# Performance work log

Hardware: AMD Instinct MI355X
Metric: run time of the kernel (lower is better)

The kernel has to match this reference:

```python
import jax, jax.numpy as jnp
import numpy as np

B, T, D = 8, 1024, 128
TEMP = 0.1
WEIGHT = 1.0


def _neg_scaled_l2(x, y):
    # x: [P, T, D], y: [P, S, D] -> -||x-y||^2 / D / TEMP  (l2 similarity, normalize_dimension=True)
    x2 = jnp.sum(x * x, axis=-1)[..., :, None]            # [P, T, 1]
    y2 = jnp.sum(y * y, axis=-1)[..., None, :]            # [P, 1, S]
    xy = jnp.einsum('ptd,psd->pts', x, y)                 # [P, T, S]
    d2 = jnp.maximum(x2 + y2 - 2.0 * xy, 0.0)             # cdist(...)**2 is non-negative
    return -d2 / D / TEMP


def setup_inputs() -> dict:
    key = jax.random.key(0)
    k1, k2, k3 = jax.random.split(key, 3)
    embs = jax.random.normal(k1, (B, T, D), dtype=jnp.float32)
    frame_idxs = jnp.sort(jax.random.randint(k2, (B, T), 0, 4096, dtype=jnp.int32), axis=-1)
    video_len = jax.random.randint(k3, (B,), T, 4096, dtype=jnp.int32)
    return {"embs": embs, "frame_idxs": frame_idxs, "video_len": video_len}


def reference(embs, frame_idxs, video_len):
    # All ordered pairs (i, j) with i != j, built at trace time.
    pairs = np.array([(i, j) for i in range(B) for j in range(B) if i != j])
    ii, jj = pairs[:, 0], pairs[:, 1]                     # [P]

    e1 = embs[ii]                                         # [P, T, D]
    e2 = embs[jj]                                         # [P, T, D]

    # Cycle: soft nearest neighbors of e1 in e2, then align back to e1.
    sim12 = _neg_scaled_l2(e1, e2)                        # [P, T, T]
    beta12 = jax.nn.softmax(sim12, axis=-1)
    nn_embs = jnp.einsum('pts,psd->ptd', beta12, e2)      # [P, T, D]
    logits = _neg_scaled_l2(nn_embs, e1)                  # [P, T, T]

    beta = jax.nn.softmax(logits, axis=-1)                # [P, T, T]
    steps = frame_idxs.astype(jnp.float32) / video_len.astype(jnp.float32)[:, None]  # [B, T]
    sp = steps[ii]                                        # [P, T] (steps of sequence i)
    time_true = sp                                        # one_hot(labels) picks the diagonal
    time_pred = jnp.einsum('pts,ps->pt', beta, sp)        # [P, T]
    loss = jnp.mean((time_pred - time_true) ** 2)
    return WEIGHT * loss
```

## Files before the change

### kernel.cpp

```cpp
#include <hip/hip_runtime.h>
#include <hip/hip_bf16.h>


#define T_ 1024
#define D_ 128
#define NPAIR 56
#define NSCALE 0.11271055006945026f
#define SQDS 0.474785316f

typedef float f32x16 __attribute__((ext_vector_type(16)));

#define B8F 131072
#define B8T 163840

__device__ __forceinline__ unsigned short f2bf(float f) {
  unsigned u = __float_as_uint(f);
  u += 0x7fff + ((u >> 16) & 1);
  return (unsigned short)(u >> 16);
}
__device__ __forceinline__ float bf2f(unsigned short v) {
  return __uint_as_float(((unsigned)v) << 16);
}
__device__ __forceinline__ float clamp8(float x) {
  return fminf(fmaxf(x, -440.f), 440.f);
}
__device__ __forceinline__ unsigned pk4(float a, float b, float c, float d) {
  int w = __builtin_amdgcn_cvt_pk_fp8_f32(a, b, 0, false);
  w = __builtin_amdgcn_cvt_pk_fp8_f32(c, d, w, true);
  return (unsigned)w;
}
__device__ __forceinline__ float waveSum(float v) {
#pragma unroll
  for (int k = 32; k >= 1; k >>= 1) v += __shfl_xor(v, k, 64);
  return v;
}

__device__ __forceinline__ void c2b8(const unsigned* m, int lh, long long* b0, long long* b1) {
  unsigned send0 = lh ? m[0] : m[1];
  unsigned send1 = lh ? m[2] : m[3];
  unsigned r0 = (unsigned)__shfl_xor((int)send0, 32, 64);
  unsigned r1 = (unsigned)__shfl_xor((int)send1, 32, 64);
  union { unsigned u[2]; long long ll; } x0, x1;
  x0.u[0] = lh ? r0 : m[0];  x0.u[1] = lh ? m[1] : r0;
  x1.u[0] = lh ? r1 : m[2];  x1.u[1] = lh ? m[3] : r1;
  *b0 = x0.ll; *b1 = x1.ll;
}

#define MFMA8(A, B, C) __builtin_amdgcn_mfma_f32_32x32x16_fp8_fp8((A), (B), (C), 0, 0, 0)
#define LD8(P, Q) (*(const long long*)((P) + (Q) * 512))
#define EXPC(x) fminf(__builtin_amdgcn_exp2f(x), 448.f)

__global__ __launch_bounds__(256) void convert_kernel(
    const float* __restrict__ embs, const int* __restrict__ fi,
    const int* __restrict__ vl, unsigned char* __restrict__ e8F,
    unsigned char* __restrict__ e8T, float* __restrict__ steps,
    float* __restrict__ acc, unsigned* __restrict__ cnt) {
  __shared__ unsigned short tileS[32 * 136];
  __shared__ float psum[32][8];
  __shared__ float g_sh[32], sp_sh[32];
  const int b = blockIdx.x >> 5;
  const int t0 = (blockIdx.x & 31) * 32;
  const int tid = threadIdx.x;
  const int row = tid >> 3, seg = tid & 7;

  if (blockIdx.x == 0 && tid == 0) { acc[0] = 0.f; cnt[0] = 0u; }

  const float* src = embs + (size_t)(b * T_ + t0 + row) * D_ + seg * 16;
  float4 g4[4];
#pragma unroll
  for (int k = 0; k < 4; k++) g4[k] = ((const float4*)src)[k];
  float s = 0.f;
  float fv[16];
#pragma unroll
  for (int k = 0; k < 4; k++) {
    s += g4[k].x * g4[k].x + g4[k].y * g4[k].y + g4[k].z * g4[k].z + g4[k].w * g4[k].w;
    fv[4 * k + 0] = g4[k].x * SQDS; fv[4 * k + 1] = g4[k].y * SQDS;
    fv[4 * k + 2] = g4[k].z * SQDS; fv[4 * k + 3] = g4[k].w * SQDS;
  }
  psum[row][seg] = s;

  {
    unsigned char* dstA = e8F + (size_t)b * B8F + (size_t)((t0 >> 5) * 8 + seg) * 512;
    uint2 lo, hi;
    lo.x = pk4(fv[0], fv[1], fv[2], fv[3]);   lo.y = pk4(fv[4], fv[5], fv[6], fv[7]);
    hi.x = pk4(fv[8], fv[9], fv[10], fv[11]); hi.y = pk4(fv[12], fv[13], fv[14], fv[15]);
    *(uint2*)(dstA + row * 8) = lo;
    *(uint2*)(dstA + (size_t)(32 + row) * 8) = hi;
  }
#pragma unroll
  for (int k = 0; k < 16; k++) tileS[row * 136 + seg * 16 + k] = f2bf(fv[k]);
  __syncthreads();

  if (tid < 32) {
    float t = 0.f;
#pragma unroll
    for (int k = 0; k < 8; k++) t += psum[tid][k];
    int gr = b * T_ + t0 + tid;
    float sp = (float)fi[gr] / (float)vl[b];
    steps[gr] = sp;
    sp_sh[tid] = sp;
    g_sh[tid] = __builtin_amdgcn_exp2f(14.0f - t * NSCALE);
  }
  __syncthreads();

  {
    const int c8 = tid >> 5;
    const int n2 = c8 & 3, scp = c8 >> 2;
    const int dd = n2 * 32 + (tid & 31);
#pragma unroll
    for (int half = 0; half < 2; half++) {
      const int lane = half * 32 + (tid & 31);
      const int sl = scp * 16 + half * 8;
      float vv[8];
#pragma unroll
      for (int jj = 0; jj < 8; jj++)
        vv[jj] = clamp8(bf2f(tileS[(sl + jj) * 136 + dd]) * g_sh[sl + jj]);
      uint2 wv;
      wv.x = pk4(vv[0], vv[1], vv[2], vv[3]);
      wv.y = pk4(vv[4], vv[5], vv[6], vv[7]);
      int c = n2 * 64 + (t0 >> 4) + scp;
      *(uint2*)(e8T + (size_t)b * B8T + (size_t)c * 512 + lane * 8) = wv;
    }
  }
  if (tid < 128) {
    const int sc2 = tid >> 6, lane = tid & 63;
    const int m = lane & 31, kh = lane >> 5;
    uint2 wv; wv.x = 0u; wv.y = 0u;
    if (m < 2) {
      float vv[8];
#pragma unroll
      for (int e = 0; e < 8; e++) {
        int sl = sc2 * 16 + kh * 8 + e;
        float gg = g_sh[sl];
        vv[e] = clamp8(m ? gg * sp_sh[sl] : gg);
      }
      wv.x = pk4(vv[0], vv[1], vv[2], vv[3]);
      wv.y = pk4(vv[4], vv[5], vv[6], vv[7]);
    }
    int c = 256 + (t0 >> 4) + sc2;
    *(uint2*)(e8T + (size_t)b * B8T + (size_t)c * 512 + lane * 8) = wv;
  }
}

__global__ __launch_bounds__(256, 2) void tcc_main(
    const unsigned char* __restrict__ e8F, const unsigned char* __restrict__ e8T,
    const float* __restrict__ steps, float* __restrict__ loss_acc,
    unsigned* __restrict__ cnt, float* __restrict__ out) {
  __shared__ float blred[4];

  const int bx = blockIdx.x;
  const int pair = bx >> 3;
  const int tile = bx & 7;
  const int i = pair / 7;
  const int r = pair % 7;
  const int j = r + (r >= i ? 1 : 0);
  const int tid = threadIdx.x;
  const int w = tid >> 6;
  const int l = tid & 63;
  const int l31 = l & 31;
  const int lh = l >> 5;
  const int tb = tile * 128 + w * 32;

  const unsigned char* eFi = e8F + (size_t)i * B8F;
  const unsigned char* eFj = e8F + (size_t)j * B8F;
  const unsigned char* eTj = e8T + (size_t)j * B8T;
  const unsigned char* eTi = e8T + (size_t)i * B8T;

  long long qf8[8];
  {
    const unsigned char* qb = eFi + (size_t)((tb >> 5) * 8) * 512 + l * 8;
#pragma unroll
    for (int kc = 0; kc < 8; kc++) qf8[kc] = LD8(qb, kc);
  }

  const f32x16 Z = {0.f, 0.f, 0.f, 0.f, 0.f, 0.f, 0.f, 0.f,
                    0.f, 0.f, 0.f, 0.f, 0.f, 0.f, 0.f, 0.f};
  const f32x16 CM6 = {-6.f, -6.f, -6.f, -6.f, -6.f, -6.f, -6.f, -6.f,
                      -6.f, -6.f, -6.f, -6.f, -6.f, -6.f, -6.f, -6.f};
  f32x16 o[5];
#pragma unroll
  for (int n2 = 0; n2 < 5; n2++) o[n2] = Z;

  for (int st = 0; st < 16; st++) {
    const unsigned char* kb = eFj + (size_t)(st * 16) * 512 + l * 8;
    const unsigned char* vb = eTj + (size_t)(st * 4) * 512 + l * 8;

    f32x16 ca0 = MFMA8(LD8(kb, 0), qf8[0], CM6);
    f32x16 ca1 = MFMA8(LD8(kb, 8), qf8[0], CM6);
#pragma unroll
    for (int dc = 1; dc < 8; dc++) {
      ca0 = MFMA8(LD8(kb, dc), qf8[dc], ca0);
      ca1 = MFMA8(LD8(kb, 8 + dc), qf8[dc], ca1);
    }
    unsigned m0[4], m1[4];
#pragma unroll
    for (int k2 = 0; k2 < 4; k2++) {
      m0[k2] = pk4(EXPC(ca0[4 * k2]), EXPC(ca0[4 * k2 + 1]),
                   EXPC(ca0[4 * k2 + 2]), EXPC(ca0[4 * k2 + 3]));
      m1[k2] = pk4(EXPC(ca1[4 * k2]), EXPC(ca1[4 * k2 + 1]),
                   EXPC(ca1[4 * k2 + 2]), EXPC(ca1[4 * k2 + 3]));
    }
    long long pB[4];
    c2b8(m0, lh, &pB[0], &pB[1]);
    c2b8(m1, lh, &pB[2], &pB[3]);
#pragma unroll
    for (int n2 = 0; n2 < 5; n2++)
#pragma unroll
      for (int sc = 0; sc < 4; sc++)
        o[n2] = MFMA8(LD8(vb, n2 * 64 + sc), pB[sc], o[n2]);
  }

  float Lme = o[4][0];
  float Lo = __shfl_xor(Lme, 32, 64);
  float inv = 1.0f / (lh ? Lo : Lme);
  long long qf2[8];
#pragma unroll
  for (int n2 = 0; n2 < 4; n2++) {
    unsigned mm[4];
#pragma unroll
    for (int k2 = 0; k2 < 4; k2++)
      mm[k2] = pk4(o[n2][4 * k2] * inv, o[n2][4 * k2 + 1] * inv,
                   o[n2][4 * k2 + 2] * inv, o[n2][4 * k2 + 3] * inv);
    c2b8(mm, lh, &qf2[2 * n2], &qf2[2 * n2 + 1]);
  }
  f32x16 acc6 = Z;

  for (int st = 0; st < 16; st++) {
    const unsigned char* kb = eFi + (size_t)(st * 16) * 512 + l * 8;
    const unsigned char* gb = eTi + (size_t)(256 + st * 4) * 512 + l * 8;

    f32x16 ca0 = MFMA8(LD8(kb, 0), qf2[0], CM6);
    f32x16 ca1 = MFMA8(LD8(kb, 8), qf2[0], CM6);
#pragma unroll
    for (int dc = 1; dc < 8; dc++) {
      ca0 = MFMA8(LD8(kb, dc), qf2[dc], ca0);
      ca1 = MFMA8(LD8(kb, 8 + dc), qf2[dc], ca1);
    }
    unsigned m0[4], m1[4];
#pragma unroll
    for (int k2 = 0; k2 < 4; k2++) {
      m0[k2] = pk4(EXPC(ca0[4 * k2]), EXPC(ca0[4 * k2 + 1]),
                   EXPC(ca0[4 * k2 + 2]), EXPC(ca0[4 * k2 + 3]));
      m1[k2] = pk4(EXPC(ca1[4 * k2]), EXPC(ca1[4 * k2 + 1]),
                   EXPC(ca1[4 * k2 + 2]), EXPC(ca1[4 * k2 + 3]));
    }
    long long pB[4];
    c2b8(m0, lh, &pB[0], &pB[1]);
    c2b8(m1, lh, &pB[2], &pB[3]);
#pragma unroll
    for (int sc = 0; sc < 4; sc++)
      acc6 = MFMA8(LD8(gb, sc), pB[sc], acc6);
  }

  float local = 0.f;
  if (lh == 0) {
    float pred = acc6[1] / acc6[0];
    float tt = steps[i * T_ + tb + l31];
    float dd = pred - tt;
    local = dd * dd;
  }
  local = waveSum(local);
  if (l == 0) blred[w] = local;
  __syncthreads();
  if (tid == 0) {
    atomicAdd(loss_acc, blred[0] + blred[1] + blred[2] + blred[3]);
    __threadfence();
    unsigned old = atomicAdd(cnt, 1u);
    if (old == (unsigned)(gridDim.x - 1)) {
      float v = atomicAdd(loss_acc, 0.0f);
      out[0] = v * (1.0f / (float)(NPAIR * T_));
    }
  }
}

extern "C" void kernel_launch(void* const* d_in, const int* in_sizes, int n_in,
                              void* d_out, int out_size, void* d_ws, size_t ws_size,
                              hipStream_t stream) {
  const float* embs = (const float*)d_in[0];
  const int* frame_idxs = (const int*)d_in[1];
  const int* video_len = (const int*)d_in[2];
  float* out = (float*)d_out;

  char* ws = (char*)d_ws;
  float* acc = (float*)ws;
  unsigned* cnt = (unsigned*)(ws + 512);
  float* steps = (float*)(ws + 4096);
  unsigned char* e8F = (unsigned char*)(ws + 65536);
  unsigned char* e8T = e8F + (size_t)8 * B8F;

  convert_kernel<<<dim3(256), dim3(256), 0, stream>>>(embs, frame_idxs, video_len,
                                                      e8F, e8T, steps, acc, cnt);
  tcc_main<<<dim3(NPAIR * 8), dim3(256), 0, stream>>>(e8F, e8T, steps, acc, cnt, out);
}
```

Baseline: 133.7 us.

## Use single-wave blocks with double-buffered async global-to-LDS staging of K/V tiles

Moves from 4-wave blocks to one wave per block (4x more blocks) and stages the fp8 key/value tiles into LDS through global_load_lds with a two-deep buffer and manual vmcnt waits, so loads overlap with MFMA and exp work. Each iteration now handles 32 keys instead of 64, and the block reduction through shared memory becomes a per-wave atomic. The cost is more atomics, hand-written waitcnt accounting that is fragile, and 18KB of LDS per single-wave block, which may limit occupancy.

New measurement: 141.3 us. 1.06x slower.

```diff
diff --git a/kernel.cpp b/kernel.cpp
--- a/kernel.cpp
+++ b/kernel.cpp
@@ -33,6 +33,11 @@
 #pragma unroll
   for (int k = 32; k >= 1; k >>= 1) v += __shfl_xor(v, k, 64);
   return v;
+}
+__device__ __forceinline__ void stage1k(const unsigned char* g, unsigned char* lds, int lane) {
+  __builtin_amdgcn_global_load_lds(
+      (const __attribute__((address_space(1))) unsigned int*)(g + lane * 16),
+      (__attribute__((address_space(3))) unsigned int*)lds, 16, 0, 0);
 }
 
 __device__ __forceinline__ void c2b8(const unsigned* m, int lh, long long* b0, long long* b1) {
@@ -49,6 +54,8 @@
 #define MFMA8(A, B, C) __builtin_amdgcn_mfma_f32_32x32x16_fp8_fp8((A), (B), (C), 0, 0, 0)
 #define LD8(P, Q) (*(const long long*)((P) + (Q) * 512))
 #define EXPC(x) fminf(__builtin_amdgcn_exp2f(x), 448.f)
+#define WAITV(N) asm volatile("s_waitcnt vmcnt(" #N ")" ::: "memory")
+#define WAITL() asm volatile("s_waitcnt lgkmcnt(0)" ::: "memory")
 
 __global__ __launch_bounds__(256) void convert_kernel(
     const float* __restrict__ embs, const int* __restrict__ fi,
@@ -142,24 +149,22 @@
   }
 }
 
-__global__ __launch_bounds__(256, 2) void tcc_main(
+__global__ __launch_bounds__(64) void tcc_main(
     const unsigned char* __restrict__ e8F, const unsigned char* __restrict__ e8T,
     const float* __restrict__ steps, float* __restrict__ loss_acc,
     unsigned* __restrict__ cnt, float* __restrict__ out) {
-  __shared__ float blred[4];
+  __shared__ unsigned char smem[18432];
 
   const int bx = blockIdx.x;
-  const int pair = bx >> 3;
-  const int tile = bx & 7;
+  const int pair = bx >> 5;
+  const int tile = bx & 31;
   const int i = pair / 7;
   const int r = pair % 7;
   const int j = r + (r >= i ? 1 : 0);
-  const int tid = threadIdx.x;
-  const int w = tid >> 6;
-  const int l = tid & 63;
+  const int l = threadIdx.x & 63;
   const int l31 = l & 31;
   const int lh = l >> 5;
-  const int tb = tile * 128 + w * 32;
+  const int tb = tile * 32;
 
   const unsigned char* eFi = e8F + (size_t)i * B8F;
   const unsigned char* eFj = e8F + (size_t)j * B8F;
@@ -168,7 +173,7 @@
 
   long long qf8[8];
   {
-    const unsigned char* qb = eFi + (size_t)((tb >> 5) * 8) * 512 + l * 8;
+    const unsigned char* qb = eFi + (size_t)(tile * 8) * 512 + l * 8;
 #pragma unroll
     for (int kc = 0; kc < 8; kc++) qf8[kc] = LD8(qb, kc);
   }
@@ -181,34 +186,59 @@
 #pragma unroll
   for (int n2 = 0; n2 < 5; n2++) o[n2] = Z;
 
-  for (int st = 0; st < 16; st++) {
-    const unsigned char* kb = eFj + (size_t)(st * 16) * 512 + l * 8;
-    const unsigned char* vb = eTj + (size_t)(st * 4) * 512 + l * 8;
-
-    f32x16 ca0 = MFMA8(LD8(kb, 0), qf8[0], CM6);
-    f32x16 ca1 = MFMA8(LD8(kb, 8), qf8[0], CM6);
-#pragma unroll
-    for (int dc = 1; dc < 8; dc++) {
-      ca0 = MFMA8(LD8(kb, dc), qf8[dc], ca0);
-      ca1 = MFMA8(LD8(kb, 8 + dc), qf8[dc], ca1);
-    }
-    unsigned m0[4], m1[4];
-#pragma unroll
-    for (int k2 = 0; k2 < 4; k2++) {
-      m0[k2] = pk4(EXPC(ca0[4 * k2]), EXPC(ca0[4 * k2 + 1]),
-                   EXPC(ca0[4 * k2 + 2]), EXPC(ca0[4 * k2 + 3]));
-      m1[k2] = pk4(EXPC(ca1[4 * k2]), EXPC(ca1[4 * k2 + 1]),
-                   EXPC(ca1[4 * k2 + 2]), EXPC(ca1[4 * k2 + 3]));
-    }
-    long long pB[4];
+  auto stg1 = [&](int t, int b) {
+    unsigned char* dst = smem + b * 9216;
+#pragma unroll
+    for (int u = 0; u < 4; u++)
+      stage1k(eFj + ((size_t)t * 8 + u * 2) * 512, dst + u * 1024, l);
+#pragma unroll
+    for (int n2 = 0; n2 < 4; n2++)
+      stage1k(eTj + ((size_t)n2 * 64 + t * 2) * 512, dst + 4096 + n2 * 1024, l);
+    stage1k(eTj + ((size_t)256 + t * 2) * 512, dst + 4096 + 4096, l);
+  };
+  auto stg2 = [&](int t, int b) {
+    unsigned char* dst = smem + b * 9216;
+#pragma unroll
+    for (int u = 0; u < 4; u++)
+      stage1k(eFi + ((size_t)t * 8 + u * 2) * 512, dst + u * 1024, l);
+    stage1k(eTi + ((size_t)256 + t * 2) * 512, dst + 4096, l);
+  };
+
+  stg1(0, 0);
+  stg1(1, 1);
+
+  for (int st = 0; st < 32; st++) {
+    const int buf = st & 1;
+    if (st == 31) { WAITV(0); } else { WAITV(9); }
+
+    const unsigned char* kb = smem + buf * 9216 + l * 8;
+    const unsigned char* vb = kb + 4096;
+
+    f32x16 ca = MFMA8(LD8(kb, 0), qf8[0], CM6);
+#pragma unroll
+    for (int dc = 1; dc < 8; dc++) ca = MFMA8(LD8(kb, dc), qf8[dc], ca);
+    unsigned m0[4];
+#pragma unroll
+    for (int k2 = 0; k2 < 4; k2++)
+      m0[k2] = pk4(EXPC(ca[4 * k2]), EXPC(ca[4 * k2 + 1]),
+                   EXPC(ca[4 * k2 + 2]), EXPC(ca[4 * k2 + 3]));
+    long long pB[2];
     c2b8(m0, lh, &pB[0], &pB[1]);
-    c2b8(m1, lh, &pB[2], &pB[3]);
 #pragma unroll
     for (int n2 = 0; n2 < 5; n2++)
 #pragma unroll
-      for (int sc = 0; sc < 4; sc++)
-        o[n2] = MFMA8(LD8(vb, n2 * 64 + sc), pB[sc], o[n2]);
-  }
+      for (int sc = 0; sc < 2; sc++)
+        o[n2] = MFMA8(LD8(vb, n2 * 2 + sc), pB[sc], o[n2]);
+
+    if (st < 30) {
+      WAITL();
+      stg1(st + 2, buf);
+    }
+  }
+
+  WAITL();
+  stg2(0, 0);
+  stg2(1, 1);
 
   float Lme = o[4][0];
   float Lo = __shfl_xor(Lme, 32, 64);
@@ -225,31 +255,31 @@
   }
   f32x16 acc6 = Z;
 
-  for (int st = 0; st < 16; st++) {
-    const unsigned char* kb = eFi + (size_t)(st * 16) * 512 + l * 8;
-    const unsigned char* gb = eTi + (size_t)(256 + st * 4) * 512 + l * 8;
-
-    f32x16 ca0 = MFMA8(LD8(kb, 0), qf2[0], CM6);
-    f32x16 ca1 = MFMA8(LD8(kb, 8), qf2[0], CM6);
-#pragma unroll
-    for (int dc = 1; dc < 8; dc++) {
-      ca0 = MFMA8(LD8(kb, dc), qf2[dc], ca0);
-      ca1 = MFMA8(LD8(kb, 8 + dc), qf2[dc], ca1);
-    }
-    unsigned m0[4], m1[4];
-#pragma unroll
-    for (int k2 = 0; k2 < 4; k2++) {
-      m0[k2] = pk4(EXPC(ca0[4 * k2]), EXPC(ca0[4 * k2 + 1]),
-                   EXPC(ca0[4 * k2 + 2]), EXPC(ca0[4 * k2 + 3]));
-      m1[k2] = pk4(EXPC(ca1[4 * k2]), EXPC(ca1[4 * k2 + 1]),
-                   EXPC(ca1[4 * k2 + 2]), EXPC(ca1[4 * k2 + 3]));
-    }
-    long long pB[4];
+  for (int st = 0; st < 32; st++) {
+    const int buf = st & 1;
+    if (st == 31) { WAITV(0); } else { WAITV(5); }
+
+    const unsigned char* kb = smem + buf * 9216 + l * 8;
+    const unsigned char* gb = kb + 4096;
+
+    f32x16 da = MFMA8(LD8(kb, 0), qf2[0], CM6);
+#pragma unroll
+    for (int dc = 1; dc < 8; dc++) da = MFMA8(LD8(kb, dc), qf2[dc], da);
+    unsigned m0[4];
+#pragma unroll
+    for (int k2 = 0; k2 < 4; k2++)
+      m0[k2] = pk4(EXPC(da[4 * k2]), EXPC(da[4 * k2 + 1]),
+                   EXPC(da[4 * k2 + 2]), EXPC(da[4 * k2 + 3]));
+    long long pB[2];
     c2b8(m0, lh, &pB[0], &pB[1]);
-    c2b8(m1, lh, &pB[2], &pB[3]);
-#pragma unroll
-    for (int sc = 0; sc < 4; sc++)
+#pragma unroll
+    for (int sc = 0; sc < 2; sc++)
       acc6 = MFMA8(LD8(gb, sc), pB[sc], acc6);
+
+    if (st < 30) {
+      WAITL();
+      stg2(st + 2, buf);
+    }
   }
 
   float local = 0.f;
@@ -260,10 +290,8 @@
     local = dd * dd;
   }
   local = waveSum(local);
-  if (l == 0) blred[w] = local;
-  __syncthreads();
-  if (tid == 0) {
-    atomicAdd(loss_acc, blred[0] + blred[1] + blred[2] + blred[3]);
+  if (l == 0) {
+    atomicAdd(loss_acc, local);
     __threadfence();
     unsigned old = atomicAdd(cnt, 1u);
     if (old == (unsigned)(gridDim.x - 1)) {
@@ -290,5 +318,5 @@
 
   convert_kernel<<<dim3(256), dim3(256), 0, stream>>>(embs, frame_idxs, video_len,
                                                       e8F, e8T, steps, acc, cnt);
-  tcc_main<<<dim3(NPAIR * 8), dim3(256), 0, stream>>>(e8F, e8T, steps, acc, cnt, out);
-}
+  tcc_main<<<dim3(NPAIR * 32), dim3(64), 0, stream>>>(e8F, e8T, steps, acc, cnt, out);
+}
```

## Stage K/V tiles into LDS with async double-buffered global_load_lds

Applied to the files above, without the earlier changes.

Main kernel now uses 128-thread blocks covering 64 query rows, doubling the grid. Key and value fp8 tiles are copied from global memory straight into a double-buffered LDS region with global_load_lds, prefetching the next step while the current one computes. MFMA sections are wrapped in setprio hints. This aims to hide global load latency and let the two waves share staged tiles, at the cost of a per-step __syncthreads, 36KB of LDS per block, and twice as many blocks reloading the same K/V data.

Measured after the change: 122.8 us. 8.2% less time.

```diff
diff --git a/kernel.cpp b/kernel.cpp
--- a/kernel.cpp
+++ b/kernel.cpp
@@ -33,6 +33,11 @@
 #pragma unroll
   for (int k = 32; k >= 1; k >>= 1) v += __shfl_xor(v, k, 64);
   return v;
+}
+__device__ __forceinline__ void stage1k(const unsigned char* g, unsigned char* lds, int lane) {
+  __builtin_amdgcn_global_load_lds(
+      (const __attribute__((address_space(1))) unsigned int*)(g + lane * 16),
+      (__attribute__((address_space(3))) unsigned int*)lds, 16, 0, 0);
 }
 
 __device__ __forceinline__ void c2b8(const unsigned* m, int lh, long long* b0, long long* b1) {
@@ -142,15 +147,19 @@
   }
 }
 
-__global__ __launch_bounds__(256, 2) void tcc_main(
+__global__ __launch_bounds__(128, 2) void tcc_main(
     const unsigned char* __restrict__ e8F, const unsigned char* __restrict__ e8T,
     const float* __restrict__ steps, float* __restrict__ loss_acc,
     unsigned* __restrict__ cnt, float* __restrict__ out) {
-  __shared__ float blred[4];
+  __shared__ unsigned char smem[36864];
+  __shared__ float blred[2];
+  unsigned char* kt = smem;
+  unsigned char* vt = smem + 16384;
+  unsigned char* gt = smem + 16384;
 
   const int bx = blockIdx.x;
-  const int pair = bx >> 3;
-  const int tile = bx & 7;
+  const int pair = bx >> 4;
+  const int tile = bx & 15;
   const int i = pair / 7;
   const int r = pair % 7;
   const int j = r + (r >= i ? 1 : 0);
@@ -159,7 +168,7 @@
   const int l = tid & 63;
   const int l31 = l & 31;
   const int lh = l >> 5;
-  const int tb = tile * 128 + w * 32;
+  const int tb = tile * 64 + w * 32;
 
   const unsigned char* eFi = e8F + (size_t)i * B8F;
   const unsigned char* eFj = e8F + (size_t)j * B8F;
@@ -181,10 +190,36 @@
 #pragma unroll
   for (int n2 = 0; n2 < 5; n2++) o[n2] = Z;
 
+  auto stageP1 = [&](int t, int b) {
+#pragma unroll
+    for (int q = 0; q < 4; q++)
+      stage1k(eFj + (size_t)(8 * t + 4 * w + q) * 1024, kt + b * 8192 + (4 * w + q) * 1024, l);
+#pragma unroll
+    for (int u = 0; u < 5; u++) {
+      int vu = w + 2 * u;
+      int n2v = vu >> 1, uh = vu & 1;
+      stage1k(eTj + (size_t)(n2v * 32 + t * 2 + uh) * 1024, vt + b * 10240 + vu * 1024, l);
+    }
+  };
+  auto stageP2 = [&](int t, int b) {
+#pragma unroll
+    for (int q = 0; q < 4; q++)
+      stage1k(eFi + (size_t)(8 * t + 4 * w + q) * 1024, kt + b * 8192 + (4 * w + q) * 1024, l);
+    stage1k(eTi + (size_t)(128 + t * 2 + w) * 1024, gt + b * 2048 + w * 1024, l);
+  };
+
+  stageP1(0, 0);
+  __syncthreads();
+
   for (int st = 0; st < 16; st++) {
-    const unsigned char* kb = eFj + (size_t)(st * 16) * 512 + l * 8;
-    const unsigned char* vb = eTj + (size_t)(st * 4) * 512 + l * 8;
-
+    const int cur = st & 1, nxt = cur ^ 1;
+    if (st < 15) stageP1(st + 1, nxt);
+    __builtin_amdgcn_sched_barrier(0);
+
+    const unsigned char* kb = kt + cur * 8192 + l * 8;
+    const unsigned char* vb = vt + cur * 10240 + l * 8;
+
+    __builtin_amdgcn_s_setprio(1);
     f32x16 ca0 = MFMA8(LD8(kb, 0), qf8[0], CM6);
     f32x16 ca1 = MFMA8(LD8(kb, 8), qf8[0], CM6);
 #pragma unroll
@@ -192,6 +227,7 @@
       ca0 = MFMA8(LD8(kb, dc), qf8[dc], ca0);
       ca1 = MFMA8(LD8(kb, 8 + dc), qf8[dc], ca1);
     }
+    __builtin_amdgcn_s_setprio(0);
     unsigned m0[4], m1[4];
 #pragma unroll
     for (int k2 = 0; k2 < 4; k2++) {
@@ -203,12 +239,17 @@
     long long pB[4];
     c2b8(m0, lh, &pB[0], &pB[1]);
     c2b8(m1, lh, &pB[2], &pB[3]);
+    __builtin_amdgcn_s_setprio(1);
 #pragma unroll
     for (int n2 = 0; n2 < 5; n2++)
 #pragma unroll
       for (int sc = 0; sc < 4; sc++)
-        o[n2] = MFMA8(LD8(vb, n2 * 64 + sc), pB[sc], o[n2]);
-  }
+        o[n2] = MFMA8(LD8(vb, n2 * 4 + sc), pB[sc], o[n2]);
+    __builtin_amdgcn_s_setprio(0);
+    __syncthreads();
+  }
+
+  stageP2(0, 0);
 
   float Lme = o[4][0];
   float Lo = __shfl_xor(Lme, 32, 64);
@@ -224,11 +265,17 @@
     c2b8(mm, lh, &qf2[2 * n2], &qf2[2 * n2 + 1]);
   }
   f32x16 acc6 = Z;
+  __syncthreads();
 
   for (int st = 0; st < 16; st++) {
-    const unsigned char* kb = eFi + (size_t)(st * 16) * 512 + l * 8;
-    const unsigned char* gb = eTi + (size_t)(256 + st * 4) * 512 + l * 8;
-
+    const int cur = st & 1, nxt = cur ^ 1;
+    if (st < 15) stageP2(st + 1, nxt);
+    __builtin_amdgcn_sched_barrier(0);
+
+    const unsigned char* kb = kt + cur * 8192 + l * 8;
+    const unsigned char* gb = gt + cur * 2048 + l * 8;
+
+    __builtin_amdgcn_s_setprio(1);
     f32x16 ca0 = MFMA8(LD8(kb, 0), qf2[0], CM6);
     f32x16 ca1 = MFMA8(LD8(kb, 8), qf2[0], CM6);
 #pragma unroll
@@ -236,6 +283,7 @@
       ca0 = MFMA8(LD8(kb, dc), qf2[dc], ca0);
       ca1 = MFMA8(LD8(kb, 8 + dc), qf2[dc], ca1);
     }
+    __builtin_amdgcn_s_setprio(0);
     unsigned m0[4], m1[4];
 #pragma unroll
     for (int k2 = 0; k2 < 4; k2++) {
@@ -247,9 +295,12 @@
     long long pB[4];
     c2b8(m0, lh, &pB[0], &pB[1]);
     c2b8(m1, lh, &pB[2], &pB[3]);
+    __builtin_amdgcn_s_setprio(1);
 #pragma unroll
     for (int sc = 0; sc < 4; sc++)
       acc6 = MFMA8(LD8(gb, sc), pB[sc], acc6);
+    __builtin_amdgcn_s_setprio(0);
+    __syncthreads();
   }
 
   float local = 0.f;
@@ -263,7 +314,7 @@
   if (l == 0) blred[w] = local;
   __syncthreads();
   if (tid == 0) {
-    atomicAdd(loss_acc, blred[0] + blred[1] + blred[2] + blred[3]);
+    atomicAdd(loss_acc, blred[0] + blred[1]);
     __threadfence();
     unsigned old = atomicAdd(cnt, 1u);
     if (old == (unsigned)(gridDim.x - 1)) {
@@ -290,5 +341,5 @@
 
   convert_kernel<<<dim3(256), dim3(256), 0, stream>>>(embs, frame_idxs, video_len,
                                                       e8F, e8T, steps, acc, cnt);
-  tcc_main<<<dim3(NPAIR * 8), dim3(256), 0, stream>>>(e8F, e8T, steps, acc, cnt, out);
-}
+  tcc_main<<<dim3(NPAIR * 16), dim3(128), 0, stream>>>(e8F, e8T, steps, acc, cnt, out);
+}
```
